# Optimization experiments

Hardware: AMD Instinct MI355X
Metric: run time of the kernel (lower is better)

The kernel has to match this reference:

```python
import jax, jax.numpy as jnp
import numpy as np

BN_EPS = 1e-5


def setup_inputs() -> dict:
    key = jax.random.key(0)
    ks = jax.random.split(key, 9)
    B, C, H, W = 2, 64, 128, 128
    Ci = 32  # inter_channels
    sc = 0.05
    x = jax.random.normal(ks[0], (B, C, H, W), jnp.float32)
    g_w = jax.random.normal(ks[1], (Ci, C), jnp.float32) * sc
    g_b = jax.random.normal(ks[2], (Ci,), jnp.float32) * sc
    theta_w = jax.random.normal(ks[3], (Ci, C), jnp.float32) * sc
    theta_b = jax.random.normal(ks[4], (Ci,), jnp.float32) * sc
    phi_w = jax.random.normal(ks[5], (Ci, C), jnp.float32) * sc
    phi_b = jax.random.normal(ks[6], (Ci,), jnp.float32) * sc
    w_w = jax.random.normal(ks[7], (C, Ci), jnp.float32) * sc
    w_b = jnp.zeros((C,), jnp.float32)
    # BatchNorm affine params (random so the block is non-trivial; the torch
    # code zero-inits them, which would make the whole block an identity).
    bn_gamma = 1.0 + 0.1 * jax.random.normal(ks[8], (C,), jnp.float32)
    bn_beta = jnp.zeros((C,), jnp.float32)
    return dict(x=x, g_w=g_w, g_b=g_b, theta_w=theta_w, theta_b=theta_b,
                phi_w=phi_w, phi_b=phi_b, w_w=w_w, w_b=w_b,
                bn_gamma=bn_gamma, bn_beta=bn_beta)


def reference(x, g_w, g_b, theta_w, theta_b, phi_w, phi_b, w_w, w_b,
              bn_gamma, bn_beta):
    B, C, H, W = x.shape
    Ci = g_w.shape[0]
    H1, W1 = H // 2, W // 2

    def block(xq):  # embedded-gaussian non-local block on one quadrant group [B,C,h,w]
        b, c, h, w = xq.shape
        n = h * w
        xf = xq.reshape(b, c, n)                                  # [B,C,N]
        th = jnp.einsum('oc,bcn->bno', theta_w, xf) + theta_b     # [B,N,Ci]
        ph = jnp.einsum('oc,bcn->bon', phi_w, xf) + phi_b[:, None]  # [B,Ci,N]
        gx = jnp.einsum('oc,bcn->bno', g_w, xf) + g_b             # [B,N,Ci]
        f = jnp.einsum('bno,bom->bnm', th, ph)                    # [B,N,N] affinity
        a = jax.nn.softmax(f, axis=-1)
        y = jnp.einsum('bnm,bmo->bno', a, gx)                     # [B,N,Ci]
        wy = jnp.einsum('co,bno->bcn', w_w, y) + w_b[:, None]     # [B,C,N]
        wy = wy.reshape(b, c, h, w)
        # BatchNorm2d, training-mode batch stats (per quadrant call in torch)
        mu = wy.mean(axis=(0, 2, 3), keepdims=True)
        var = wy.var(axis=(0, 2, 3), keepdims=True)
        bn = (wy - mu) * jax.lax.rsqrt(var + BN_EPS)
        bn = bn * bn_gamma[None, :, None, None] + bn_beta[None, :, None, None]
        return bn + xq                                            # residual

    # split into 4 quadrants: [B,C,H,W] -> [4,B,C,H1,W1] (quadrant-major)
    xq = x.reshape(B, C, 2, H1, 2, W1).transpose(2, 4, 0, 1, 3, 5)
    xq = xq.reshape(4, B, C, H1, W1)
    zq = jax.vmap(block)(xq)                                      # [4,B,C,H1,W1]
    # reassemble
    z = zq.reshape(2, 2, B, C, H1, W1).transpose(2, 3, 0, 4, 1, 5)
    return z.reshape(B, C, H, W)
```

## Files before the change

kernel.cpp:

```cpp
#include <hip/hip_runtime.h>
#include <stdint.h>

typedef __bf16 bf16x8 __attribute__((ext_vector_type(8)));
typedef short  short4v __attribute__((ext_vector_type(4)));
typedef float  floatx4 __attribute__((ext_vector_type(4)));
typedef uint32_t u32x4 __attribute__((ext_vector_type(4)));

#define DI __device__ __forceinline__

DI uint16_t bf1(float a) {
    union { __bf16 h; uint16_t u; } r; r.h = (__bf16)a; return r.u;
}

__global__ __launch_bounds__(256) void proj_kernel(
    const float* __restrict__ x,
    const float* __restrict__ tw, const float* __restrict__ tb,
    const float* __restrict__ pw, const float* __restrict__ pb,
    const float* __restrict__ gw, const float* __restrict__ gb,
    uint16_t* __restrict__ th, uint16_t* __restrict__ phT,
    uint16_t* __restrict__ vP)
{
    __shared__ uint16_t ldsg[32 * 68];
    int blk = blockIdx.x & 7, nt = blockIdx.x >> 3;
    int tid = threadIdx.x, wid = tid >> 6, lane = tid & 63;
    int quad = lane >> 4, low = lane & 15;

    int b = blk & 1, q = blk >> 1, qh = q >> 1, qw = q & 1;
    int pixA = wid * 16 + low;
    const float* xg = x + (size_t)b * 1048576 +
                      (size_t)(qh * 64 + nt) * 128 + qw * 64 + pixA;

    float a0[8], a1[8];
#pragma unroll
    for (int j = 0; j < 8; ++j) {
        a0[j] = xg[(size_t)(quad * 8 + j) * 16384];
        a1[j] = xg[(size_t)(32 + quad * 8 + j) * 16384];
    }
    bf16x8 A0, A1;
#pragma unroll
    for (int j = 0; j < 8; ++j) {
        A0[j] = (__bf16)a0[j];
        A1[j] = (__bf16)a1[j];
    }

    auto dotile = [&](const float* W, const float* Bv, int o0) -> floatx4 {
        floatx4 acc;
        float bias = Bv[o0 + low];
#pragma unroll
        for (int r = 0; r < 4; ++r) acc[r] = bias;
        const float* wr = W + (o0 + low) * 64 + quad * 8;
        floatx4 w0a = *(const floatx4*)(wr);
        floatx4 w0b = *(const floatx4*)(wr + 4);
        floatx4 w1a = *(const floatx4*)(wr + 32);
        floatx4 w1b = *(const floatx4*)(wr + 36);
        bf16x8 B0, B1;
#pragma unroll
        for (int j = 0; j < 4; ++j) {
            B0[j]     = (__bf16)w0a[j];
            B0[j + 4] = (__bf16)w0b[j];
            B1[j]     = (__bf16)w1a[j];
            B1[j + 4] = (__bf16)w1b[j];
        }
        acc = __builtin_amdgcn_mfma_f32_16x16x32_bf16(A0, B0, acc, 0, 0, 0);
        acc = __builtin_amdgcn_mfma_f32_16x16x32_bf16(A1, B1, acc, 0, 0, 0);
        return acc;
    };

    size_t thbase = ((size_t)blk * 4096 + nt * 64 + wid * 16 + quad * 4) * 32;

    floatx4 t0 = dotile(tw, tb, 0), t1 = dotile(tw, tb, 16);
#pragma unroll
    for (int r = 0; r < 4; ++r) {
        th[thbase + r * 32 + low]      = bf1(t0[r] * 1.44269504088896f);
        th[thbase + r * 32 + 16 + low] = bf1(t1[r] * 1.44269504088896f);
    }
    floatx4 p0 = dotile(pw, pb, 0), p1 = dotile(pw, pb, 16);
#pragma unroll
    for (int r = 0; r < 4; ++r) {
        phT[thbase + r * 32 + low]      = bf1(p0[r]);
        phT[thbase + r * 32 + 16 + low] = bf1(p1[r]);
    }
    floatx4 g0 = dotile(gw, gb, 0), g1 = dotile(gw, gb, 16);
#pragma unroll
    for (int r = 0; r < 4; ++r) {
        ldsg[(low)      * 68 + wid * 16 + quad * 4 + r] = bf1(g0[r]);
        ldsg[(16 + low) * 68 + wid * 16 + quad * 4 + r] = bf1(g1[r]);
    }
    __syncthreads();
    {
        int o = tid >> 3, k = (tid & 7) * 8;
        const uint16_t* src = &ldsg[o * 68 + k];
        uint64_t lo = *(const uint64_t*)(src);
        uint64_t hi = *(const uint64_t*)(src + 4);
        union { uint64_t q[2]; u32x4 v; } out;
        out.q[0] = lo; out.q[1] = hi;
        *(u32x4*)(vP + (size_t)blk * 131072 + nt * 2048 + tid * 8) = out.v;
    }
}

__global__ __launch_bounds__(512, 4) void flash_kernel(
    const uint16_t* __restrict__ th, const uint16_t* __restrict__ phT,
    const uint16_t* __restrict__ vP, const float* __restrict__ w_w,
    const float* __restrict__ w_b, float* __restrict__ wy,
    float2* __restrict__ partials)
{
    __shared__ uint16_t ldsK[4][2][64 * 40];
    __shared__ uint16_t ldsV[4][2][32 * 72];
    __shared__ float sred[2][64][2];
    int blk = blockIdx.x & 7;
    int rg  = blockIdx.x >> 3;
    int tid = threadIdx.x, wid = tid >> 6, lane = tid & 63;
    int sp = wid >> 1, qg = wid & 1;
    int lt = tid & 127;
    int quad = lane >> 4, low = lane & 15;
    int n0 = rg * 64 + qg * 32;

    const uint16_t* thB = th  + (size_t)blk * 131072;
    const uint16_t* kG  = phT + (size_t)blk * 131072;
    const uint16_t* vG  = vP  + (size_t)blk * 131072;

    bf16x8 qfA = *(const bf16x8*)(thB + (n0 + low) * 32 + quad * 8);
    bf16x8 qfB = *(const bf16x8*)(thB + (n0 + 16 + low) * 32 + quad * 8);

    const u32x4* kSrc = (const u32x4*)kG + sp * 4096 + lt;
    const u32x4* vSrc = (const u32x4*)vG + sp * 4096 + lt;
    const int kW0 = ((lt >> 2)) * 40 + (lt & 3) * 8;
    const int kW1 = (32 + (lt >> 2)) * 40 + (lt & 3) * 8;
    const int vW0 = ((lt >> 3)) * 72 + (lt & 7) * 8;
    const int vW1 = (16 + (lt >> 3)) * 72 + (lt & 7) * 8;

    u32x4 kr0 = kSrc[0], kr1 = kSrc[128];
    u32x4 vr0 = vSrc[0], vr1 = vSrc[128];
    *(u32x4*)(&ldsK[sp][0][kW0]) = kr0;  *(u32x4*)(&ldsK[sp][0][kW1]) = kr1;
    *(u32x4*)(&ldsV[sp][0][vW0]) = vr0;  *(u32x4*)(&ldsV[sp][0][vW1]) = vr1;
    __syncthreads();

    floatx4 zero = {0.f, 0.f, 0.f, 0.f};
    floatx4 oaA0 = zero, oaA1 = zero, osA = zero;
    floatx4 oaB0 = zero, oaB1 = zero, osB = zero;
    union { uint32_t u[4]; bf16x8 v; } ones8;
    ones8.u[0] = 0x3F803F80u; ones8.u[1] = 0x3F803F80u;
    ones8.u[2] = 0x3F803F80u; ones8.u[3] = 0x3F803F80u;

    for (int t = 0; t < 16; ++t) {
        int buf = t & 1;
        if (t < 15) {
            kr0 = kSrc[(t + 1) * 256];  kr1 = kSrc[(t + 1) * 256 + 128];
            vr0 = vSrc[(t + 1) * 256];  vr1 = vSrc[(t + 1) * 256 + 128];
        }
        const uint16_t* Kb = ldsK[sp][buf];
        const uint16_t* Vb = ldsV[sp][buf];
        bf16x8 kf[4];
        union { short4v s[2]; bf16x8 v; } vA2[2], vB2[2];
#pragma unroll
        for (int c = 0; c < 4; ++c)
            kf[c] = *(const bf16x8*)(Kb + (c * 16 + low) * 40 + quad * 8);
#pragma unroll
        for (int c2 = 0; c2 < 2; ++c2) {
            vA2[c2].s[0] = *(const short4v*)(Vb + low * 72 + (2*c2)     * 16 + quad * 4);
            vA2[c2].s[1] = *(const short4v*)(Vb + low * 72 + (2*c2 + 1) * 16 + quad * 4);
            vB2[c2].s[0] = *(const short4v*)(Vb + (16 + low) * 72 + (2*c2)     * 16 + quad * 4);
            vB2[c2].s[1] = *(const short4v*)(Vb + (16 + low) * 72 + (2*c2 + 1) * 16 + quad * 4);
        }
        {
            floatx4 sa[4];
#pragma unroll
            for (int c = 0; c < 4; ++c)
                sa[c] = __builtin_amdgcn_mfma_f32_16x16x32_bf16(kf[c], qfA, zero, 0, 0, 0);
            union { __bf16 h[8]; bf16x8 v; } P2[2];
#pragma unroll
            for (int c2 = 0; c2 < 2; ++c2) {
#pragma unroll
                for (int j = 0; j < 4; ++j) {
                    P2[c2].h[j]     = (__bf16)__builtin_amdgcn_exp2f(sa[2*c2][j]);
                    P2[c2].h[4 + j] = (__bf16)__builtin_amdgcn_exp2f(sa[2*c2 + 1][j]);
                }
            }
#pragma unroll
            for (int c2 = 0; c2 < 2; ++c2) {
                oaA0 = __builtin_amdgcn_mfma_f32_16x16x32_bf16(vA2[c2].v, P2[c2].v, oaA0, 0, 0, 0);
                oaA1 = __builtin_amdgcn_mfma_f32_16x16x32_bf16(vB2[c2].v, P2[c2].v, oaA1, 0, 0, 0);
                osA  = __builtin_amdgcn_mfma_f32_16x16x32_bf16(ones8.v,   P2[c2].v, osA,  0, 0, 0);
            }
        }
        {
            floatx4 sa[4];
#pragma unroll
            for (int c = 0; c < 4; ++c)
                sa[c] = __builtin_amdgcn_mfma_f32_16x16x32_bf16(kf[c], qfB, zero, 0, 0, 0);
            union { __bf16 h[8]; bf16x8 v; } P2[2];
#pragma unroll
            for (int c2 = 0; c2 < 2; ++c2) {
#pragma unroll
                for (int j = 0; j < 4; ++j) {
                    P2[c2].h[j]     = (__bf16)__builtin_amdgcn_exp2f(sa[2*c2][j]);
                    P2[c2].h[4 + j] = (__bf16)__builtin_amdgcn_exp2f(sa[2*c2 + 1][j]);
                }
            }
#pragma unroll
            for (int c2 = 0; c2 < 2; ++c2) {
                oaB0 = __builtin_amdgcn_mfma_f32_16x16x32_bf16(vA2[c2].v, P2[c2].v, oaB0, 0, 0, 0);
                oaB1 = __builtin_amdgcn_mfma_f32_16x16x32_bf16(vB2[c2].v, P2[c2].v, oaB1, 0, 0, 0);
                osB  = __builtin_amdgcn_mfma_f32_16x16x32_bf16(ones8.v,   P2[c2].v, osB,  0, 0, 0);
            }
        }
        if (t < 15) {
            *(u32x4*)(&ldsK[sp][buf ^ 1][kW0]) = kr0;
            *(u32x4*)(&ldsK[sp][buf ^ 1][kW1]) = kr1;
            *(u32x4*)(&ldsV[sp][buf ^ 1][vW0]) = vr0;
            *(u32x4*)(&ldsV[sp][buf ^ 1][vW1]) = vr1;
        }
        __syncthreads();
    }

    {
        float* exW = (float*)(&ldsK[0][0][0]);
        int li = tid * 18;
#pragma unroll
        for (int r = 0; r < 4; ++r) {
            exW[li + r]      = oaA0[r];
            exW[li + 4 + r]  = oaA1[r];
            exW[li + 9 + r]  = oaB0[r];
            exW[li + 13 + r] = oaB1[r];
        }
        exW[li + 8]  = osA[0];
        exW[li + 17] = osB[0];
    }
    __syncthreads();
    floatx4 cA0 = zero, cA1 = zero, cB0 = zero, cB1 = zero;
    float cosA = 0.f, cosB = 0.f;
    {
        const float* exR = (const float*)(&ldsK[0][0][0]);
#pragma unroll
        for (int s = 0; s < 4; ++s) {
            const float* p = exR + (s * 128 + lt) * 18;
#pragma unroll
            for (int r = 0; r < 4; ++r) {
                cA0[r] += p[r];
                cA1[r] += p[4 + r];
                cB0[r] += p[9 + r];
                cB1[r] += p[13 + r];
            }
            cosA += p[8];
            cosB += p[17];
        }
    }

    float rinvA = 1.0f / cosA, rinvB = 1.0f / cosB;
    union { __bf16 h[8]; bf16x8 v; } YA8, YB8;
#pragma unroll
    for (int r = 0; r < 4; ++r) {
        YA8.h[r]     = (__bf16)(cA0[r] * rinvA);
        YA8.h[4 + r] = (__bf16)(cA1[r] * rinvA);
        YB8.h[r]     = (__bf16)(cB0[r] * rinvB);
        YB8.h[4 + r] = (__bf16)(cB1[r] * rinvB);
    }

    float* wyB = wy + (size_t)blk * 262144;
    int nA = n0 + low, nB = n0 + 16 + low;
    int ct = sp;
    {
        floatx4 accA, accB;
#pragma unroll
        for (int r = 0; r < 4; ++r) {
            accA[r] = w_b[ct * 16 + quad * 4 + r];
            accB[r] = accA[r];
        }
        floatx4 w0 = *(const floatx4*)(w_w + (ct * 16 + low) * 32 + quad * 4);
        floatx4 w1 = *(const floatx4*)(w_w + (ct * 16 + low) * 32 + 16 + quad * 4);
        union { __bf16 h[8]; bf16x8 v; } W8;
#pragma unroll
        for (int r = 0; r < 4; ++r) {
            W8.h[r]     = (__bf16)w0[r];
            W8.h[4 + r] = (__bf16)w1[r];
        }
        accA = __builtin_amdgcn_mfma_f32_16x16x32_bf16(W8.v, YA8.v, accA, 0, 0, 0);
        accB = __builtin_amdgcn_mfma_f32_16x16x32_bf16(W8.v, YB8.v, accB, 0, 0, 0);
#pragma unroll
        for (int r = 0; r < 4; ++r) {
            int ch = ct * 16 + quad * 4 + r;
            wyB[(size_t)ch * 4096 + nA] = accA[r];
            wyB[(size_t)ch * 4096 + nB] = accB[r];
            float s = accA[r] + accB[r];
            float ss = accA[r] * accA[r] + accB[r] * accB[r];
            s += __shfl_xor(s, 1); ss += __shfl_xor(ss, 1);
            s += __shfl_xor(s, 2); ss += __shfl_xor(ss, 2);
            s += __shfl_xor(s, 4); ss += __shfl_xor(ss, 4);
            s += __shfl_xor(s, 8); ss += __shfl_xor(ss, 8);
            if (low == 0) {
                sred[qg][ch][0] = s;
                sred[qg][ch][1] = ss;
            }
        }
    }
    __syncthreads();
    if (tid < 64) {
        float s  = sred[0][tid][0] + sred[1][tid][0];
        float ss = sred[0][tid][1] + sred[1][tid][1];
        partials[((size_t)blk * 64 + rg) * 64 + tid] = make_float2(s, ss);
    }
}

__global__ __launch_bounds__(64) void stats_kernel(
    const float2* __restrict__ partials, const float* __restrict__ gamma,
    const float* __restrict__ beta, float2* __restrict__ stats)
{
    int q = blockIdx.x >> 6, c = blockIdx.x & 63;
    int t = threadIdx.x;
    float2 p0 = partials[(((size_t)(q * 2 + 0)) * 64 + t) * 64 + c];
    float2 p1 = partials[(((size_t)(q * 2 + 1)) * 64 + t) * 64 + c];
    float S = p0.x + p1.x, SS = p0.y + p1.y;
    S += __shfl_xor(S, 1);  SS += __shfl_xor(SS, 1);
    S += __shfl_xor(S, 2);  SS += __shfl_xor(SS, 2);
    S += __shfl_xor(S, 4);  SS += __shfl_xor(SS, 4);
    S += __shfl_xor(S, 8);  SS += __shfl_xor(SS, 8);
    S += __shfl_xor(S, 16); SS += __shfl_xor(SS, 16);
    S += __shfl_xor(S, 32); SS += __shfl_xor(SS, 32);
    if (t == 0) {
        float mu  = S * (1.0f / 8192.0f);
        float var = SS * (1.0f / 8192.0f) - mu * mu;
        float scale = gamma[c] * rsqrtf(var + 1e-5f);
        float shift = beta[c] - mu * scale;
        stats[q * 64 + c] = make_float2(scale, shift);
    }
}

__global__ __launch_bounds__(256) void final_kernel(
    const float* __restrict__ wy, const float2* __restrict__ stats,
    const float* __restrict__ x, float* __restrict__ out)
{
    int bid = blockIdx.x;
    size_t base = (((size_t)(bid & 7) * 256 + (bid >> 3)) * 256 + threadIdx.x) * 4;
    int n   = (int)(base & 4095);
    int c   = (int)((base >> 12) & 63);
    int blk = (int)(base >> 18);
    int b = blk & 1, q = blk >> 1, qh = q >> 1, qw = q & 1;
    int i = n >> 6, j = n & 63;
    float2 sc = stats[q * 64 + c];
    floatx4 wv = *(const floatx4*)(wy + base);
    size_t xa = ((size_t)(b * 64 + c) * 128 + (qh * 64 + i)) * 128 + qw * 64 + j;
    floatx4 xv = *(const floatx4*)(x + xa);
    floatx4 ov;
#pragma unroll
    for (int k = 0; k < 4; ++k) ov[k] = wv[k] * sc.x + sc.y + xv[k];
    *(floatx4*)(out + xa) = ov;
}

extern "C" void kernel_launch(void* const* d_in, const int* in_sizes, int n_in,
                              void* d_out, int out_size, void* d_ws, size_t ws_size,
                              hipStream_t stream)
{
    const float* x       = (const float*)d_in[0];
    const float* g_w     = (const float*)d_in[1];
    const float* g_b     = (const float*)d_in[2];
    const float* theta_w = (const float*)d_in[3];
    const float* theta_b = (const float*)d_in[4];
    const float* phi_w   = (const float*)d_in[5];
    const float* phi_b   = (const float*)d_in[6];
    const float* w_w     = (const float*)d_in[7];
    const float* w_b     = (const float*)d_in[8];
    const float* gamma   = (const float*)d_in[9];
    const float* beta    = (const float*)d_in[10];

    char* ws = (char*)d_ws;
    uint16_t* th       = (uint16_t*)(ws);
    uint16_t* phT      = (uint16_t*)(ws + (2u << 20));
    uint16_t* vP       = (uint16_t*)(ws + (4u << 20));
    float*    wy       = (float*)(ws + (6u << 20));
    float2*   partials = (float2*)(ws + (14u << 20));
    float2*   stats    = (float2*)(ws + (14u << 20) + (1u << 18));

    proj_kernel  <<<512,  256, 0, stream>>>(x, theta_w, theta_b, phi_w, phi_b,
                                            g_w, g_b, th, phT, vP);
    flash_kernel <<<512,  512, 0, stream>>>(th, phT, vP, w_w, w_b, wy, partials);
    stats_kernel <<<256,  64,  0, stream>>>(partials, gamma, beta, stats);
    final_kernel <<<2048, 256, 0, stream>>>(wy, stats, x, (float*)d_out);
}
```

Baseline: 123.3 us.

## Load K/V MFMA fragments directly from global memory, drop LDS staging

The flash kernel no longer stages K and V tiles through double-buffered shared memory with a barrier per tile. Each wave now loads its MFMA operand fragments straight from global memory into registers, using a two-register-set software pipeline. The projection kernel's V write layout is permuted so each lane's 8-element fragment is contiguous. This removes LDS traffic and per-iteration barriers, at the cost of more register pressure and redundant global/L2 reads across the waves that share a split.

```diff
diff --git a/kernel.cpp b/kernel.cpp
--- a/kernel.cpp
+++ b/kernel.cpp
@@ -88,10 +88,11 @@
     }
     __syncthreads();
     {
-        int o = tid >> 3, k = (tid & 7) * 8;
-        const uint16_t* src = &ldsg[o * 68 + k];
+        int o = tid >> 3, f = tid & 7;
+        int c2 = f >> 2, qd = f & 3;
+        const uint16_t* src = &ldsg[o * 68 + c2 * 32 + qd * 4];
         uint64_t lo = *(const uint64_t*)(src);
-        uint64_t hi = *(const uint64_t*)(src + 4);
+        uint64_t hi = *(const uint64_t*)(src + 16);
         union { uint64_t q[2]; u32x4 v; } out;
         out.q[0] = lo; out.q[1] = hi;
         *(u32x4*)(vP + (size_t)blk * 131072 + nt * 2048 + tid * 8) = out.v;
@@ -104,8 +105,7 @@
     const float* __restrict__ w_b, float* __restrict__ wy,
     float2* __restrict__ partials)
 {
-    __shared__ uint16_t ldsK[4][2][64 * 40];
-    __shared__ uint16_t ldsV[4][2][32 * 72];
+    __shared__ float exbuf[512 * 18];
     __shared__ float sred[2][64][2];
     int blk = blockIdx.x & 7;
     int rg  = blockIdx.x >> 3;
@@ -122,18 +122,8 @@
     bf16x8 qfA = *(const bf16x8*)(thB + (n0 + low) * 32 + quad * 8);
     bf16x8 qfB = *(const bf16x8*)(thB + (n0 + 16 + low) * 32 + quad * 8);
 
-    const u32x4* kSrc = (const u32x4*)kG + sp * 4096 + lt;
-    const u32x4* vSrc = (const u32x4*)vG + sp * 4096 + lt;
-    const int kW0 = ((lt >> 2)) * 40 + (lt & 3) * 8;
-    const int kW1 = (32 + (lt >> 2)) * 40 + (lt & 3) * 8;
-    const int vW0 = ((lt >> 3)) * 72 + (lt & 7) * 8;
-    const int vW1 = (16 + (lt >> 3)) * 72 + (lt & 7) * 8;
-
-    u32x4 kr0 = kSrc[0], kr1 = kSrc[128];
-    u32x4 vr0 = vSrc[0], vr1 = vSrc[128];
-    *(u32x4*)(&ldsK[sp][0][kW0]) = kr0;  *(u32x4*)(&ldsK[sp][0][kW1]) = kr1;
-    *(u32x4*)(&ldsV[sp][0][vW0]) = vr0;  *(u32x4*)(&ldsV[sp][0][vW1]) = vr1;
-    __syncthreads();
+    const uint16_t* kBase = kG + (size_t)(sp * 1024 + low) * 32 + quad * 8;
+    const uint16_t* vBase = vG + (size_t)sp * 32768 + low * 64 + quad * 8;
 
     floatx4 zero = {0.f, 0.f, 0.f, 0.f};
     floatx4 oaA0 = zero, oaA1 = zero, osA = zero;
@@ -142,108 +132,95 @@
     ones8.u[0] = 0x3F803F80u; ones8.u[1] = 0x3F803F80u;
     ones8.u[2] = 0x3F803F80u; ones8.u[3] = 0x3F803F80u;
 
-    for (int t = 0; t < 16; ++t) {
-        int buf = t & 1;
-        if (t < 15) {
-            kr0 = kSrc[(t + 1) * 256];  kr1 = kSrc[(t + 1) * 256 + 128];
-            vr0 = vSrc[(t + 1) * 256];  vr1 = vSrc[(t + 1) * 256 + 128];
-        }
-        const uint16_t* Kb = ldsK[sp][buf];
-        const uint16_t* Vb = ldsV[sp][buf];
-        bf16x8 kf[4];
-        union { short4v s[2]; bf16x8 v; } vA2[2], vB2[2];
-#pragma unroll
-        for (int c = 0; c < 4; ++c)
-            kf[c] = *(const bf16x8*)(Kb + (c * 16 + low) * 40 + quad * 8);
-#pragma unroll
-        for (int c2 = 0; c2 < 2; ++c2) {
-            vA2[c2].s[0] = *(const short4v*)(Vb + low * 72 + (2*c2)     * 16 + quad * 4);
-            vA2[c2].s[1] = *(const short4v*)(Vb + low * 72 + (2*c2 + 1) * 16 + quad * 4);
-            vB2[c2].s[0] = *(const short4v*)(Vb + (16 + low) * 72 + (2*c2)     * 16 + quad * 4);
-            vB2[c2].s[1] = *(const short4v*)(Vb + (16 + low) * 72 + (2*c2 + 1) * 16 + quad * 4);
-        }
-        {
-            floatx4 sa[4];
-#pragma unroll
-            for (int c = 0; c < 4; ++c)
-                sa[c] = __builtin_amdgcn_mfma_f32_16x16x32_bf16(kf[c], qfA, zero, 0, 0, 0);
-            union { __bf16 h[8]; bf16x8 v; } P2[2];
-#pragma unroll
-            for (int c2 = 0; c2 < 2; ++c2) {
-#pragma unroll
-                for (int j = 0; j < 4; ++j) {
-                    P2[c2].h[j]     = (__bf16)__builtin_amdgcn_exp2f(sa[2*c2][j]);
-                    P2[c2].h[4 + j] = (__bf16)__builtin_amdgcn_exp2f(sa[2*c2 + 1][j]);
-                }
-            }
-#pragma unroll
-            for (int c2 = 0; c2 < 2; ++c2) {
-                oaA0 = __builtin_amdgcn_mfma_f32_16x16x32_bf16(vA2[c2].v, P2[c2].v, oaA0, 0, 0, 0);
-                oaA1 = __builtin_amdgcn_mfma_f32_16x16x32_bf16(vB2[c2].v, P2[c2].v, oaA1, 0, 0, 0);
-                osA  = __builtin_amdgcn_mfma_f32_16x16x32_bf16(ones8.v,   P2[c2].v, osA,  0, 0, 0);
-            }
-        }
-        {
-            floatx4 sa[4];
-#pragma unroll
-            for (int c = 0; c < 4; ++c)
-                sa[c] = __builtin_amdgcn_mfma_f32_16x16x32_bf16(kf[c], qfB, zero, 0, 0, 0);
-            union { __bf16 h[8]; bf16x8 v; } P2[2];
-#pragma unroll
-            for (int c2 = 0; c2 < 2; ++c2) {
-#pragma unroll
-                for (int j = 0; j < 4; ++j) {
-                    P2[c2].h[j]     = (__bf16)__builtin_amdgcn_exp2f(sa[2*c2][j]);
-                    P2[c2].h[4 + j] = (__bf16)__builtin_amdgcn_exp2f(sa[2*c2 + 1][j]);
-                }
-            }
-#pragma unroll
-            for (int c2 = 0; c2 < 2; ++c2) {
-                oaB0 = __builtin_amdgcn_mfma_f32_16x16x32_bf16(vA2[c2].v, P2[c2].v, oaB0, 0, 0, 0);
-                oaB1 = __builtin_amdgcn_mfma_f32_16x16x32_bf16(vB2[c2].v, P2[c2].v, oaB1, 0, 0, 0);
-                osB  = __builtin_amdgcn_mfma_f32_16x16x32_bf16(ones8.v,   P2[c2].v, osB,  0, 0, 0);
-            }
-        }
-        if (t < 15) {
-            *(u32x4*)(&ldsK[sp][buf ^ 1][kW0]) = kr0;
-            *(u32x4*)(&ldsK[sp][buf ^ 1][kW1]) = kr1;
-            *(u32x4*)(&ldsV[sp][buf ^ 1][vW0]) = vr0;
-            *(u32x4*)(&ldsV[sp][buf ^ 1][vW1]) = vr1;
-        }
-        __syncthreads();
-    }
+    bf16x8 kfA0, kfA1, kfA2, kfA3, vaA0, vaA1, vbA0, vbA1;
+    bf16x8 kfB0, kfB1, kfB2, kfB3, vaB0, vaB1, vbB0, vbB1;
+
+#define LOADT(K0, K1, K2, K3, VA0, VA1, VB0, VB1, T) {                        \
+        const uint16_t* kp = kBase + (T) * 2048;                              \
+        const uint16_t* vp = vBase + (T) * 2048;                              \
+        K0 = *(const bf16x8*)(kp);                                            \
+        K1 = *(const bf16x8*)(kp + 512);                                      \
+        K2 = *(const bf16x8*)(kp + 1024);                                     \
+        K3 = *(const bf16x8*)(kp + 1536);                                     \
+        VA0 = *(const bf16x8*)(vp);                                           \
+        VA1 = *(const bf16x8*)(vp + 32);                                      \
+        VB0 = *(const bf16x8*)(vp + 1024);                                    \
+        VB1 = *(const bf16x8*)(vp + 1056);                                    \
+    }
+
+#define COMPUTET(K0, K1, K2, K3, VA0, VA1, VB0, VB1) {                        \
+        floatx4 saA[4], saB[4];                                               \
+        saA[0] = __builtin_amdgcn_mfma_f32_16x16x32_bf16(K0, qfA, zero, 0, 0, 0); \
+        saA[1] = __builtin_amdgcn_mfma_f32_16x16x32_bf16(K1, qfA, zero, 0, 0, 0); \
+        saA[2] = __builtin_amdgcn_mfma_f32_16x16x32_bf16(K2, qfA, zero, 0, 0, 0); \
+        saA[3] = __builtin_amdgcn_mfma_f32_16x16x32_bf16(K3, qfA, zero, 0, 0, 0); \
+        saB[0] = __builtin_amdgcn_mfma_f32_16x16x32_bf16(K0, qfB, zero, 0, 0, 0); \
+        saB[1] = __builtin_amdgcn_mfma_f32_16x16x32_bf16(K1, qfB, zero, 0, 0, 0); \
+        saB[2] = __builtin_amdgcn_mfma_f32_16x16x32_bf16(K2, qfB, zero, 0, 0, 0); \
+        saB[3] = __builtin_amdgcn_mfma_f32_16x16x32_bf16(K3, qfB, zero, 0, 0, 0); \
+        union { __bf16 h[8]; bf16x8 v; } PA[2], PB[2];                        \
+        _Pragma("unroll")                                                     \
+        for (int c2 = 0; c2 < 2; ++c2) {                                      \
+            _Pragma("unroll")                                                 \
+            for (int j = 0; j < 4; ++j) {                                     \
+                PA[c2].h[j]     = (__bf16)__builtin_amdgcn_exp2f(saA[2*c2][j]);     \
+                PA[c2].h[4 + j] = (__bf16)__builtin_amdgcn_exp2f(saA[2*c2 + 1][j]); \
+                PB[c2].h[j]     = (__bf16)__builtin_amdgcn_exp2f(saB[2*c2][j]);     \
+                PB[c2].h[4 + j] = (__bf16)__builtin_amdgcn_exp2f(saB[2*c2 + 1][j]); \
+            }                                                                 \
+        }                                                                     \
+        oaA0 = __builtin_amdgcn_mfma_f32_16x16x32_bf16(VA0, PA[0].v, oaA0, 0, 0, 0); \
+        oaA1 = __builtin_amdgcn_mfma_f32_16x16x32_bf16(VB0, PA[0].v, oaA1, 0, 0, 0); \
+        osA  = __builtin_amdgcn_mfma_f32_16x16x32_bf16(ones8.v, PA[0].v, osA, 0, 0, 0); \
+        oaA0 = __builtin_amdgcn_mfma_f32_16x16x32_bf16(VA1, PA[1].v, oaA0, 0, 0, 0); \
+        oaA1 = __builtin_amdgcn_mfma_f32_16x16x32_bf16(VB1, PA[1].v, oaA1, 0, 0, 0); \
+        osA  = __builtin_amdgcn_mfma_f32_16x16x32_bf16(ones8.v, PA[1].v, osA, 0, 0, 0); \
+        oaB0 = __builtin_amdgcn_mfma_f32_16x16x32_bf16(VA0, PB[0].v, oaB0, 0, 0, 0); \
+        oaB1 = __builtin_amdgcn_mfma_f32_16x16x32_bf16(VB0, PB[0].v, oaB1, 0, 0, 0); \
+        osB  = __builtin_amdgcn_mfma_f32_16x16x32_bf16(ones8.v, PB[0].v, osB, 0, 0, 0); \
+        oaB0 = __builtin_amdgcn_mfma_f32_16x16x32_bf16(VA1, PB[1].v, oaB0, 0, 0, 0); \
+        oaB1 = __builtin_amdgcn_mfma_f32_16x16x32_bf16(VB1, PB[1].v, oaB1, 0, 0, 0); \
+        osB  = __builtin_amdgcn_mfma_f32_16x16x32_bf16(ones8.v, PB[1].v, osB, 0, 0, 0); \
+    }
+
+    LOADT(kfA0, kfA1, kfA2, kfA3, vaA0, vaA1, vbA0, vbA1, 0);
+    for (int t = 0; t < 16; t += 2) {
+        LOADT(kfB0, kfB1, kfB2, kfB3, vaB0, vaB1, vbB0, vbB1, t + 1);
+        COMPUTET(kfA0, kfA1, kfA2, kfA3, vaA0, vaA1, vbA0, vbA1);
+        if (t < 14)
+            LOADT(kfA0, kfA1, kfA2, kfA3, vaA0, vaA1, vbA0, vbA1, t + 2);
+        COMPUTET(kfB0, kfB1, kfB2, kfB3, vaB0, vaB1, vbB0, vbB1);
+    }
+#undef LOADT
+#undef COMPUTET
 
     {
-        float* exW = (float*)(&ldsK[0][0][0]);
         int li = tid * 18;
 #pragma unroll
         for (int r = 0; r < 4; ++r) {
-            exW[li + r]      = oaA0[r];
-            exW[li + 4 + r]  = oaA1[r];
-            exW[li + 9 + r]  = oaB0[r];
-            exW[li + 13 + r] = oaB1[r];
-        }
-        exW[li + 8]  = osA[0];
-        exW[li + 17] = osB[0];
+            exbuf[li + r]      = oaA0[r];
+            exbuf[li + 4 + r]  = oaA1[r];
+            exbuf[li + 9 + r]  = oaB0[r];
+            exbuf[li + 13 + r] = oaB1[r];
+        }
+        exbuf[li + 8]  = osA[0];
+        exbuf[li + 17] = osB[0];
     }
     __syncthreads();
     floatx4 cA0 = zero, cA1 = zero, cB0 = zero, cB1 = zero;
     float cosA = 0.f, cosB = 0.f;
-    {
-        const float* exR = (const float*)(&ldsK[0][0][0]);
-#pragma unroll
-        for (int s = 0; s < 4; ++s) {
-            const float* p = exR + (s * 128 + lt) * 18;
-#pragma unroll
-            for (int r = 0; r < 4; ++r) {
-                cA0[r] += p[r];
-                cA1[r] += p[4 + r];
-                cB0[r] += p[9 + r];
-                cB1[r] += p[13 + r];
-            }
-            cosA += p[8];
-            cosB += p[17];
-        }
+#pragma unroll
+    for (int s = 0; s < 4; ++s) {
+        const float* p = exbuf + (s * 128 + lt) * 18;
+#pragma unroll
+        for (int r = 0; r < 4; ++r) {
+            cA0[r] += p[r];
+            cA1[r] += p[4 + r];
+            cB0[r] += p[9 + r];
+            cB1[r] += p[13 + r];
+        }
+        cosA += p[8];
+        cosB += p[17];
     }
 
     float rinvA = 1.0f / cosA, rinvB = 1.0f / cosB;
```

New measurement: 143.0 us. +16.0%, slower.
